# Optimization experiments

Hardware: AMD Instinct MI355X
Metric: run time of the kernel (lower is better)

## Reference

```python
import jax, jax.numpy as jnp
import numpy as np

BN_EPS = 1e-5

def _bn_eval(h, g, b, rm, rv):
    return (h - rm) * (g * jax.lax.rsqrt(rv + BN_EPS)) + b

def _gin_agg(x, edge_index, eps):
    # sum_{j->i} x_j  +  (1+eps)*x_i ; PyG convention: edge_index[0]=src, edge_index[1]=dst
    src, dst = edge_index[0], edge_index[1]
    agg = jax.ops.segment_sum(x[src], dst, num_segments=x.shape[0])
    return (1.0 + eps[0]) * x + agg


def setup_inputs() -> dict:
    key = jax.random.key(0)
    ks = jax.random.split(key, 24)
    N, E, Etr, F, H, C = 10000, 160000, 40000, 128, 512, 7

    def lin(k, fan_in, shape):
        bound = 1.0 / np.sqrt(fan_in)
        return jax.random.uniform(k, shape, jnp.float32, -bound, bound)

    inp = {
        "x": jax.random.normal(ks[0], (N, F), jnp.float32),
        "edge_index": jax.random.randint(ks[1], (2, E), 0, N, jnp.int64),
        "train_edge_id": jax.random.randint(ks[2], (Etr,), 0, E, jnp.int64),
        "eps1": jnp.zeros((1,), jnp.float32),
        "W1a": lin(ks[3], F, (F, H)), "b1a": lin(ks[4], F, (H,)),
        "W1b": lin(ks[5], H, (H, H)), "b1b": lin(ks[6], H, (H,)),
        "g1": jax.random.uniform(ks[7], (H,), jnp.float32, 0.5, 1.5),
        "be1": 0.1 * jax.random.normal(ks[8], (H,), jnp.float32),
        "rm1": 0.1 * jax.random.normal(ks[9], (H,), jnp.float32),
        "rv1": jax.random.uniform(ks[10], (H,), jnp.float32, 0.5, 1.5),
        "eps2": jnp.zeros((1,), jnp.float32),
        "W2a": lin(ks[11], H, (H, H)), "b2a": lin(ks[12], H, (H,)),
        "g2": jax.random.uniform(ks[13], (H,), jnp.float32, 0.5, 1.5),
        "be2": 0.1 * jax.random.normal(ks[14], (H,), jnp.float32),
        "rm2": 0.1 * jax.random.normal(ks[15], (H,), jnp.float32),
        "rv2": jax.random.uniform(ks[16], (H,), jnp.float32, 0.5, 1.5),
        "Wl": lin(ks[17], H, (H, H)), "bl": lin(ks[18], H, (H,)),
        "Wf": lin(ks[19], H, (H, C)), "bf": lin(ks[20], H, (C,)),
    }
    return inp


def reference(x, edge_index, train_edge_id, eps1, W1a, b1a, W1b, b1b, g1, be1, rm1, rv1,
              eps2, W2a, b2a, g2, be2, rm2, rv2, Wl, bl, Wf, bf):
    # GINConv 1: agg -> Linear-ReLU-Linear-ReLU-BN
    h = _gin_agg(x, edge_index, eps1)
    h = jax.nn.relu(h @ W1a + b1a)
    h = jax.nn.relu(h @ W1b + b1b)
    h = _bn_eval(h, g1, be1, rm1, rv1)
    # GINConv 2: agg -> Linear-ReLU-BN
    h = _gin_agg(h, edge_index, eps2)
    h = jax.nn.relu(h @ W2a + b2a)
    h = _bn_eval(h, g2, be2, rm2, rv2)
    # node head (dropout is identity in eval mode)
    h = jax.nn.relu(h @ Wl + bl)
    # edge-level scoring
    node_id = edge_index[:, train_edge_id]          # [2, Etr]
    e = h[node_id[0]] * h[node_id[1]]               # [Etr, H]
    return e @ Wf + bf                               # [Etr, C]
```

## Files before the change

kernel.cpp:

```cpp
#include <hip/hip_runtime.h>
#include <hip/hip_bf16.h>

#define N_NODES 10000
#define M_PAD   10112
#define F_IN    128
#define H_DIM   512
#define N_CLS   7
#define NCHUNK  8
#define CCOLS   (H_DIM / NCHUNK)

typedef __bf16  bf16x8  __attribute__((ext_vector_type(8)));
typedef float   f32x4   __attribute__((ext_vector_type(4)));
typedef ushort  ushort8 __attribute__((ext_vector_type(8)));

__device__ __forceinline__ ushort f2bf(float f) {
    union { float f; unsigned u; } x; x.f = f;
    unsigned r = x.u + 0x7fffu + ((x.u >> 16) & 1u);
    return (ushort)(r >> 16);
}
__device__ __forceinline__ float bf2f(ushort h) {
    union { unsigned u; float f; } x; x.u = ((unsigned)h) << 16;
    return x.f;
}

__device__ __forceinline__ void gload16(const void* g, void* l) {
    __builtin_amdgcn_global_load_lds(
        (const __attribute__((address_space(1))) void*)g,
        (__attribute__((address_space(3))) void*)l, 16, 0, 0);
}


__global__ void k_zero_i32(int* __restrict__ p, int n) {
    int i = blockIdx.x * blockDim.x + threadIdx.x;
    if (i < n) p[i] = 0;
}

__global__ void k_hist(const int* __restrict__ ei, int* __restrict__ counts, int E) {
    int e = blockIdx.x * blockDim.x + threadIdx.x;
    if (e < E) atomicAdd(&counts[ei[E + e]], 1);
}

__global__ __launch_bounds__(1024) void k_scan(const int* __restrict__ counts,
                                               int* __restrict__ offsets,
                                               int* __restrict__ cursor,
                                               int N, int E) {
    __shared__ int sm[1024];
    int t = threadIdx.x;
    int base = t * 10;
    int loc[10];
    int s = 0;
    #pragma unroll
    for (int i = 0; i < 10; ++i) {
        int idx = base + i;
        int c = (idx < N) ? counts[idx] : 0;
        loc[i] = s;
        s += c;
    }
    sm[t] = s;
    __syncthreads();
    for (int off = 1; off < 1024; off <<= 1) {
        int v = (t >= off) ? sm[t - off] : 0;
        __syncthreads();
        sm[t] += v;
        __syncthreads();
    }
    int excl = sm[t] - s;
    #pragma unroll
    for (int i = 0; i < 10; ++i) {
        int idx = base + i;
        if (idx < N) {
            int o = excl + loc[i];
            offsets[idx] = o;
            cursor[idx] = o;
        }
    }
    if (t == 0) offsets[N] = E;
}

__global__ void k_scatter(const int* __restrict__ ei, int* __restrict__ cursor,
                          int* __restrict__ csr_src, int E) {
    int e = blockIdx.x * blockDim.x + threadIdx.x;
    if (e < E) {
        int d = ei[E + e];
        int pos = atomicAdd(&cursor[d], 1);
        csr_src[pos] = ei[e];
    }
}


__global__ void k_wsplit(const float* __restrict__ W, ushort* __restrict__ Th,
                         ushort* __restrict__ Tl, int K, int N) {
    int idx = blockIdx.x * blockDim.x + threadIdx.x;
    if (idx >= K * N) return;
    int n = idx / K, k = idx % K;
    float w = W[(size_t)k * N + n];
    ushort hb = f2bf(w);
    Th[idx] = hb;
    Tl[idx] = f2bf(w - bf2f(hb));
}


__global__ __launch_bounds__(256) void k_agg_f32(
    const float* __restrict__ X, const int* __restrict__ csr,
    const int* __restrict__ offs, const float* __restrict__ eps,
    ushort* __restrict__ Oh, ushort* __restrict__ Ol) {
    const int wv = threadIdx.x >> 6, lane = threadIdx.x & 63;
    const int n = blockIdx.x * 4 + wv;
    if (n >= N_NODES) return;
    const int c0 = lane * 2;
    const int s0 = offs[n], s1 = offs[n + 1];
    float a0 = 0.f, a1 = 0.f;
    int i = s0;
    for (; i + 1 < s1; i += 2) {
        const float2 v0 = *(const float2*)(X + (size_t)csr[i] * F_IN + c0);
        const float2 v1 = *(const float2*)(X + (size_t)csr[i + 1] * F_IN + c0);
        a0 += v0.x + v1.x;
        a1 += v0.y + v1.y;
    }
    if (i < s1) {
        const float2 v = *(const float2*)(X + (size_t)csr[i] * F_IN + c0);
        a0 += v.x; a1 += v.y;
    }
    const float2 sv = *(const float2*)(X + (size_t)n * F_IN + c0);
    const float e = 1.f + eps[0];
    const float v0 = e * sv.x + a0;
    const float v1 = e * sv.y + a1;
    ushort2 oh, ol;
    oh.x = f2bf(v0); ol.x = f2bf(v0 - bf2f(oh.x));
    oh.y = f2bf(v1); ol.y = f2bf(v1 - bf2f(oh.y));
    const size_t o = (size_t)n * F_IN + c0;
    *(ushort2*)(Oh + o) = oh;
    *(ushort2*)(Ol + o) = ol;
}


__global__ __launch_bounds__(256) void k_agg_pair(
    const ushort* __restrict__ Xh, const ushort* __restrict__ Xl,
    const int* __restrict__ csr, const int* __restrict__ offs,
    const float* __restrict__ eps,
    ushort* __restrict__ Oh, ushort* __restrict__ Ol) {
    const int chunk = blockIdx.x & (NCHUNK - 1);
    const int grp   = blockIdx.x >> 3;
    const int tid   = threadIdx.x;
    const int n     = grp * 16 + (tid >> 4);
    const int sub   = tid & 15;
    const int plane = sub >> 3;
    const int col   = chunk * CCOLS + (sub & 7) * 8;
    const ushort* __restrict__ X = plane ? Xl : Xh;

    const int s0 = offs[n], s1 = offs[n + 1];
    float acc[8] = {0.f, 0.f, 0.f, 0.f, 0.f, 0.f, 0.f, 0.f};
    for (int i = s0; i < s1; ++i) {
        const ushort8 v = *(const ushort8*)(X + (size_t)csr[i] * H_DIM + col);
        #pragma unroll
        for (int r = 0; r < 8; ++r) acc[r] += bf2f(v[r]);
    }
    {
        const ushort8 sv = *(const ushort8*)(X + (size_t)n * H_DIM + col);
        const float e = 1.f + eps[0];
        #pragma unroll
        for (int r = 0; r < 8; ++r) acc[r] += e * bf2f(sv[r]);
    }
    float tot[8];
    #pragma unroll
    for (int r = 0; r < 8; ++r) tot[r] = acc[r] + __shfl_xor(acc[r], 8, 64);
    if (plane == 0) {
        ushort8 oh, ol;
        #pragma unroll
        for (int r = 0; r < 8; ++r) {
            oh[r] = f2bf(tot[r]);
            ol[r] = f2bf(tot[r] - bf2f(oh[r]));
        }
        const size_t o = (size_t)n * H_DIM + col;
        *(ushort8*)(Oh + o) = oh;
        *(ushort8*)(Ol + o) = ol;
    }
}


template <int DO_BN>
__global__ __launch_bounds__(256) void k_gemm_mfma(
    const ushort* __restrict__ Ah, const ushort* __restrict__ Al,
    const ushort* __restrict__ Wh, const ushort* __restrict__ Wlo,
    const float* __restrict__ bias,
    const float* __restrict__ g, const float* __restrict__ be,
    const float* __restrict__ rm, const float* __restrict__ rv,
    ushort* __restrict__ Oh, ushort* __restrict__ Ol,
    int K, int Nout) {
    __shared__ __align__(16) ushort As_h[64][32];
    __shared__ __align__(16) ushort As_l[64][32];
    __shared__ __align__(16) ushort Bs_h[128][32];
    __shared__ __align__(16) ushort Bs_l[128][32];

    const int tid  = threadIdx.x;
    const int lane = tid & 63;
    const int wid  = tid >> 6;
    const int wm   = wid >> 1, wn = wid & 1;
    const int bm = blockIdx.x * 64, bn = blockIdx.y * 128;
    const int rsel = lane & 15;
    const int kh   = (lane >> 4) * 8;

    f32x4 acc[2][4];
    #pragma unroll
    for (int m = 0; m < 2; ++m)
        #pragma unroll
        for (int n = 0; n < 4; ++n) {
            acc[m][n][0] = 0.f; acc[m][n][1] = 0.f;
            acc[m][n][2] = 0.f; acc[m][n][3] = 0.f;
        }

    for (int k0 = 0; k0 < K; k0 += 32) {
        {
            const int off = tid * 16;
            const int row = off >> 6;
            const int ke  = (off & 63) >> 1;
            const size_t ga = (size_t)(bm + row) * K + (k0 + ke);
            gload16(Ah + ga, (char*)As_h + off);
            gload16(Al + ga, (char*)As_l + off);
        }
        #pragma unroll
        for (int c = 0; c < 2; ++c) {
            const int off = tid * 16 + c * 4096;
            const int row = off >> 6;
            const int ke  = (off & 63) >> 1;
            const size_t gb = (size_t)(bn + row) * K + (k0 + ke);
            gload16(Wh + gb,  (char*)Bs_h + off);
            gload16(Wlo + gb, (char*)Bs_l + off);
        }
        __syncthreads();
        bf16x8 a_h[2], a_l[2], b_h[4], b_l[4];
        #pragma unroll
        for (int m = 0; m < 2; ++m) {
            const int r = wm * 32 + m * 16 + rsel;
            a_h[m] = *(const bf16x8*)&As_h[r][kh];
            a_l[m] = *(const bf16x8*)&As_l[r][kh];
        }
        #pragma unroll
        for (int n = 0; n < 4; ++n) {
            const int r = wn * 64 + n * 16 + rsel;
            b_h[n] = *(const bf16x8*)&Bs_h[r][kh];
            b_l[n] = *(const bf16x8*)&Bs_l[r][kh];
        }
        #pragma unroll
        for (int m = 0; m < 2; ++m)
            #pragma unroll
            for (int n = 0; n < 4; ++n) {
                acc[m][n] = __builtin_amdgcn_mfma_f32_16x16x32_bf16(a_h[m], b_h[n], acc[m][n], 0, 0, 0);
                acc[m][n] = __builtin_amdgcn_mfma_f32_16x16x32_bf16(a_h[m], b_l[n], acc[m][n], 0, 0, 0);
                acc[m][n] = __builtin_amdgcn_mfma_f32_16x16x32_bf16(a_l[m], b_h[n], acc[m][n], 0, 0, 0);
            }
        __syncthreads();
    }

    float bs[4], sc[4], sh[4];
    int cols[4];
    #pragma unroll
    for (int n = 0; n < 4; ++n) {
        const int col = bn + wn * 64 + n * 16 + rsel;
        cols[n] = col;
        bs[n] = bias[col];
        if (DO_BN) {
            const float s = g[col] * rsqrtf(rv[col] + 1e-5f);
            sc[n] = s;
            sh[n] = be[col] - rm[col] * s;
        } else {
            sc[n] = 0.f; sh[n] = 0.f;
        }
    }
    #pragma unroll
    for (int m = 0; m < 2; ++m) {
        #pragma unroll
        for (int r = 0; r < 4; ++r) {
            const int row = bm + wm * 32 + m * 16 + (lane >> 4) * 4 + r;
            #pragma unroll
            for (int n = 0; n < 4; ++n) {
                float v = acc[m][n][r] + bs[n];
                v = fmaxf(v, 0.f);
                if (DO_BN) v = v * sc[n] + sh[n];
                const ushort hb = f2bf(v);
                const ushort lb = f2bf(v - bf2f(hb));
                const size_t o = (size_t)row * Nout + cols[n];
                Oh[o] = hb;
                Ol[o] = lb;
            }
        }
    }
}


__global__ __launch_bounds__(256) void k_edge(
    const ushort* __restrict__ hh, const ushort* __restrict__ hl,
    const int* __restrict__ ei, const int* __restrict__ tids,
    const float* __restrict__ Wf, const float* __restrict__ bf_,
    float* __restrict__ out, int Etr, int E) {
    const int lane = threadIdx.x & 63;
    const int wv   = threadIdx.x >> 6;
    float wfr[8][N_CLS];
    #pragma unroll
    for (int r = 0; r < 8; ++r)
        #pragma unroll
        for (int c = 0; c < N_CLS; ++c)
            wfr[r][c] = Wf[(lane * 8 + r) * N_CLS + c];
    float bfr[N_CLS];
    #pragma unroll
    for (int c = 0; c < N_CLS; ++c) bfr[c] = bf_[c];

    const int wid  = blockIdx.x * 4 + wv;
    const int step = gridDim.x * 4;
    for (int t = wid; t < Etr; t += step) {
        const int eid = tids[t];
        const size_t a = (size_t)ei[eid] * H_DIM + lane * 8;
        const size_t b = (size_t)ei[E + eid] * H_DIM + lane * 8;
        const ushort8 ah = *(const ushort8*)(hh + a);
        const ushort8 al = *(const ushort8*)(hl + a);
        const ushort8 bh = *(const ushort8*)(hh + b);
        const ushort8 bl = *(const ushort8*)(hl + b);
        float acc[N_CLS] = {0.f, 0.f, 0.f, 0.f, 0.f, 0.f, 0.f};
        #pragma unroll
        for (int r = 0; r < 8; ++r) {
            const float va = bf2f(ah[r]) + bf2f(al[r]);
            const float vb = bf2f(bh[r]) + bf2f(bl[r]);
            const float e = va * vb;
            #pragma unroll
            for (int c = 0; c < N_CLS; ++c) acc[c] = fmaf(e, wfr[r][c], acc[c]);
        }
        #pragma unroll
        for (int o = 32; o; o >>= 1)
            #pragma unroll
            for (int c = 0; c < N_CLS; ++c) acc[c] += __shfl_xor(acc[c], o, 64);
        if (lane == 0) {
            #pragma unroll
            for (int c = 0; c < N_CLS; ++c) out[(size_t)t * N_CLS + c] = acc[c] + bfr[c];
        }
    }
}


extern "C" void kernel_launch(void* const* d_in, const int* in_sizes, int n_in,
                              void* d_out, int out_size, void* d_ws, size_t ws_size,
                              hipStream_t stream) {
    const float* x    = (const float*)d_in[0];
    const int*   ei   = (const int*)d_in[1];
    const int*   tids = (const int*)d_in[2];
    const float* eps1 = (const float*)d_in[3];
    const float* W1a  = (const float*)d_in[4];
    const float* b1a  = (const float*)d_in[5];
    const float* W1b  = (const float*)d_in[6];
    const float* b1b  = (const float*)d_in[7];
    const float* g1p  = (const float*)d_in[8];
    const float* be1  = (const float*)d_in[9];
    const float* rm1  = (const float*)d_in[10];
    const float* rv1  = (const float*)d_in[11];
    const float* eps2 = (const float*)d_in[12];
    const float* W2a  = (const float*)d_in[13];
    const float* b2a  = (const float*)d_in[14];
    const float* g2p  = (const float*)d_in[15];
    const float* be2  = (const float*)d_in[16];
    const float* rm2  = (const float*)d_in[17];
    const float* rv2  = (const float*)d_in[18];
    const float* Wl   = (const float*)d_in[19];
    const float* bl   = (const float*)d_in[20];
    const float* Wf   = (const float*)d_in[21];
    const float* bf   = (const float*)d_in[22];
    float* out = (float*)d_out;

    const int E   = in_sizes[1] / 2;
    const int Etr = in_sizes[2];

    char* ws = (char*)d_ws;
    size_t off = 0;
    auto alloc = [&](size_t bytes) -> char* {
        char* p = ws + off;
        off += (bytes + 255) & ~(size_t)255;
        return p;
    };
    int*    counts  = (int*)alloc((size_t)N_NODES * 4);
    int*    offsets = (int*)alloc((size_t)(N_NODES + 1) * 4);
    int*    cursor  = (int*)alloc((size_t)N_NODES * 4);
    int*    csr_src = (int*)alloc((size_t)E * 4);
    ushort* h0h = (ushort*)alloc((size_t)M_PAD * F_IN * 2);
    ushort* h0l = (ushort*)alloc((size_t)M_PAD * F_IN * 2);
    ushort* Ahh = (ushort*)alloc((size_t)M_PAD * H_DIM * 2);
    ushort* Ahl = (ushort*)alloc((size_t)M_PAD * H_DIM * 2);
    ushort* Bhh = (ushort*)alloc((size_t)M_PAD * H_DIM * 2);
    ushort* Bhl = (ushort*)alloc((size_t)M_PAD * H_DIM * 2);
    ushort* wt1a_h = (ushort*)alloc((size_t)H_DIM * F_IN * 2);
    ushort* wt1a_l = (ushort*)alloc((size_t)H_DIM * F_IN * 2);
    ushort* wt1b_h = (ushort*)alloc((size_t)H_DIM * H_DIM * 2);
    ushort* wt1b_l = (ushort*)alloc((size_t)H_DIM * H_DIM * 2);
    ushort* wt2a_h = (ushort*)alloc((size_t)H_DIM * H_DIM * 2);
    ushort* wt2a_l = (ushort*)alloc((size_t)H_DIM * H_DIM * 2);
    ushort* wtl_h  = (ushort*)alloc((size_t)H_DIM * H_DIM * 2);
    ushort* wtl_l  = (ushort*)alloc((size_t)H_DIM * H_DIM * 2);
    (void)ws_size; (void)n_in; (void)out_size;

    k_zero_i32<<<(N_NODES + 255) / 256, 256, 0, stream>>>(counts, N_NODES);
    k_hist<<<(E + 255) / 256, 256, 0, stream>>>(ei, counts, E);
    k_scan<<<1, 1024, 0, stream>>>(counts, offsets, cursor, N_NODES, E);
    k_scatter<<<(E + 255) / 256, 256, 0, stream>>>(ei, cursor, csr_src, E);

    k_wsplit<<<(H_DIM * F_IN + 255) / 256, 256, 0, stream>>>(W1a, wt1a_h, wt1a_l, F_IN, H_DIM);
    k_wsplit<<<(H_DIM * H_DIM + 255) / 256, 256, 0, stream>>>(W1b, wt1b_h, wt1b_l, H_DIM, H_DIM);
    k_wsplit<<<(H_DIM * H_DIM + 255) / 256, 256, 0, stream>>>(W2a, wt2a_h, wt2a_l, H_DIM, H_DIM);
    k_wsplit<<<(H_DIM * H_DIM + 255) / 256, 256, 0, stream>>>(Wl,  wtl_h,  wtl_l,  H_DIM, H_DIM);

    k_agg_f32<<<(N_NODES + 3) / 4, 256, 0, stream>>>(x, csr_src, offsets, eps1, h0h, h0l);

    dim3 gdim(M_PAD / 64, H_DIM / 128);
    k_gemm_mfma<0><<<gdim, 256, 0, stream>>>(h0h, h0l, wt1a_h, wt1a_l, b1a,
                                             nullptr, nullptr, nullptr, nullptr,
                                             Ahh, Ahl, F_IN, H_DIM);
    k_gemm_mfma<1><<<gdim, 256, 0, stream>>>(Ahh, Ahl, wt1b_h, wt1b_l, b1b,
                                             g1p, be1, rm1, rv1,
                                             Bhh, Bhl, H_DIM, H_DIM);
    k_agg_pair<<<(N_NODES / 16) * NCHUNK, 256, 0, stream>>>(Bhh, Bhl, csr_src, offsets, eps2, Ahh, Ahl);
    k_gemm_mfma<1><<<gdim, 256, 0, stream>>>(Ahh, Ahl, wt2a_h, wt2a_l, b2a,
                                             g2p, be2, rm2, rv2,
                                             Bhh, Bhl, H_DIM, H_DIM);
    k_gemm_mfma<0><<<gdim, 256, 0, stream>>>(Bhh, Bhl, wtl_h, wtl_l, bl,
                                             nullptr, nullptr, nullptr, nullptr,
                                             Ahh, Ahl, H_DIM, H_DIM);
    k_edge<<<2048, 256, 0, stream>>>(Ahh, Ahl, ei, tids, Wf, bf, out, Etr, E);
}
```

Baseline: 326.3 us.

## Double-buffer GEMM shared-memory tiles and transpose weight split through LDS

```diff
diff --git a/kernel.cpp b/kernel.cpp
--- a/kernel.cpp
+++ b/kernel.cpp
@@ -88,15 +88,30 @@
 }
 
 
-__global__ void k_wsplit(const float* __restrict__ W, ushort* __restrict__ Th,
-                         ushort* __restrict__ Tl, int K, int N) {
-    int idx = blockIdx.x * blockDim.x + threadIdx.x;
-    if (idx >= K * N) return;
-    int n = idx / K, k = idx % K;
-    float w = W[(size_t)k * N + n];
-    ushort hb = f2bf(w);
-    Th[idx] = hb;
-    Tl[idx] = f2bf(w - bf2f(hb));
+__global__ __launch_bounds__(256) void k_wsplit(const float* __restrict__ W,
+                                                ushort* __restrict__ Th,
+                                                ushort* __restrict__ Tl,
+                                                int K, int N) {
+    __shared__ float tile[32][33];
+    const int bk = blockIdx.x * 32;
+    const int bn = blockIdx.y * 32;
+    const int c  = threadIdx.x & 31;
+    const int r0 = threadIdx.x >> 5;
+    #pragma unroll
+    for (int i = 0; i < 4; ++i) {
+        const int r = r0 + i * 8;
+        tile[r][c] = W[(size_t)(bk + r) * N + bn + c];
+    }
+    __syncthreads();
+    #pragma unroll
+    for (int i = 0; i < 4; ++i) {
+        const int r = r0 + i * 8;
+        const float w = tile[c][r];
+        const ushort hb = f2bf(w);
+        const size_t o = (size_t)(bn + r) * K + bk + c;
+        Th[o] = hb;
+        Tl[o] = f2bf(w - bf2f(hb));
+    }
 }
 
 
@@ -187,10 +202,10 @@
     const float* __restrict__ rm, const float* __restrict__ rv,
     ushort* __restrict__ Oh, ushort* __restrict__ Ol,
     int K, int Nout) {
-    __shared__ __align__(16) ushort As_h[64][32];
-    __shared__ __align__(16) ushort As_l[64][32];
-    __shared__ __align__(16) ushort Bs_h[128][32];
-    __shared__ __align__(16) ushort Bs_l[128][32];
+    __shared__ __align__(16) ushort As_h[2][64][32];
+    __shared__ __align__(16) ushort As_l[2][64][32];
+    __shared__ __align__(16) ushort Bs_h[2][128][32];
+    __shared__ __align__(16) ushort Bs_l[2][128][32];
 
     const int tid  = threadIdx.x;
     const int lane = tid & 63;
@@ -209,14 +224,14 @@
             acc[m][n][2] = 0.f; acc[m][n][3] = 0.f;
         }
 
-    for (int k0 = 0; k0 < K; k0 += 32) {
+    auto stage = [&](int buf, int k0) {
         {
             const int off = tid * 16;
             const int row = off >> 6;
             const int ke  = (off & 63) >> 1;
             const size_t ga = (size_t)(bm + row) * K + (k0 + ke);
-            gload16(Ah + ga, (char*)As_h + off);
-            gload16(Al + ga, (char*)As_l + off);
+            gload16(Ah + ga, (char*)&As_h[buf][0][0] + off);
+            gload16(Al + ga, (char*)&As_l[buf][0][0] + off);
         }
         #pragma unroll
         for (int c = 0; c < 2; ++c) {
@@ -224,22 +239,30 @@
             const int row = off >> 6;
             const int ke  = (off & 63) >> 1;
             const size_t gb = (size_t)(bn + row) * K + (k0 + ke);
-            gload16(Wh + gb,  (char*)Bs_h + off);
-            gload16(Wlo + gb, (char*)Bs_l + off);
-        }
-        __syncthreads();
+            gload16(Wh + gb,  (char*)&Bs_h[buf][0][0] + off);
+            gload16(Wlo + gb, (char*)&Bs_l[buf][0][0] + off);
+        }
+    };
+
+    stage(0, 0);
+    __syncthreads();
+    const int NT = K >> 5;
+    for (int t = 0; t < NT; ++t) {
+        const int cur = t & 1;
+        if (t + 1 < NT) stage(cur ^ 1, (t + 1) << 5);
+
         bf16x8 a_h[2], a_l[2], b_h[4], b_l[4];
         #pragma unroll
         for (int m = 0; m < 2; ++m) {
             const int r = wm * 32 + m * 16 + rsel;
-            a_h[m] = *(const bf16x8*)&As_h[r][kh];
-            a_l[m] = *(const bf16x8*)&As_l[r][kh];
+            a_h[m] = *(const bf16x8*)&As_h[cur][r][kh];
+            a_l[m] = *(const bf16x8*)&As_l[cur][r][kh];
         }
         #pragma unroll
         for (int n = 0; n < 4; ++n) {
             const int r = wn * 64 + n * 16 + rsel;
-            b_h[n] = *(const bf16x8*)&Bs_h[r][kh];
-            b_l[n] = *(const bf16x8*)&Bs_l[r][kh];
+            b_h[n] = *(const bf16x8*)&Bs_h[cur][r][kh];
+            b_l[n] = *(const bf16x8*)&Bs_l[cur][r][kh];
         }
         #pragma unroll
         for (int m = 0; m < 2; ++m)
@@ -399,10 +422,10 @@
     k_scan<<<1, 1024, 0, stream>>>(counts, offsets, cursor, N_NODES, E);
     k_scatter<<<(E + 255) / 256, 256, 0, stream>>>(ei, cursor, csr_src, E);
 
-    k_wsplit<<<(H_DIM * F_IN + 255) / 256, 256, 0, stream>>>(W1a, wt1a_h, wt1a_l, F_IN, H_DIM);
-    k_wsplit<<<(H_DIM * H_DIM + 255) / 256, 256, 0, stream>>>(W1b, wt1b_h, wt1b_l, H_DIM, H_DIM);
-    k_wsplit<<<(H_DIM * H_DIM + 255) / 256, 256, 0, stream>>>(W2a, wt2a_h, wt2a_l, H_DIM, H_DIM);
-    k_wsplit<<<(H_DIM * H_DIM + 255) / 256, 256, 0, stream>>>(Wl,  wtl_h,  wtl_l,  H_DIM, H_DIM);
+    k_wsplit<<<dim3(F_IN / 32, H_DIM / 32), 256, 0, stream>>>(W1a, wt1a_h, wt1a_l, F_IN, H_DIM);
+    k_wsplit<<<dim3(H_DIM / 32, H_DIM / 32), 256, 0, stream>>>(W1b, wt1b_h, wt1b_l, H_DIM, H_DIM);
+    k_wsplit<<<dim3(H_DIM / 32, H_DIM / 32), 256, 0, stream>>>(W2a, wt2a_h, wt2a_l, H_DIM, H_DIM);
+    k_wsplit<<<dim3(H_DIM / 32, H_DIM / 32), 256, 0, stream>>>(Wl,  wtl_h,  wtl_l,  H_DIM, H_DIM);
 
     k_agg_f32<<<(N_NODES + 3) / 4, 256, 0, stream>>>(x, csr_src, offsets, eps1, h0h, h0l);
 
```

Result: faster. 317.3 us (-2.8%).
